# Kernel optimization log

Hardware: AMD Instinct MI355X
Metric: run time of the kernel (lower is better)

Reference implementation:

```python
import jax, jax.numpy as jnp
import numpy as np
import math

B, S, D, H = 2, 2048, 2048, 16
DH = D // H  # head dim = 128
THETA = 10000.0


def _rope(x, pos):
    """Interleaved RoPE. x: [..., S, DH], pos: [S] (int)."""
    dh = x.shape[-1]
    freqs = (1.0 / THETA) ** (2.0 * jnp.arange(dh // 2, dtype=jnp.float32) / dh)  # [DH/2]
    ang = pos.astype(jnp.float32)[:, None] * freqs[None, :]  # [S, DH/2]
    cos = jnp.cos(ang).astype(x.dtype)
    sin = jnp.sin(ang).astype(x.dtype)
    xe = x[..., 0::2]
    xo = x[..., 1::2]
    oe = xe * cos - xo * sin
    oo = xe * sin + xo * cos
    return jnp.stack([oe, oo], axis=-1).reshape(x.shape)


def setup_inputs() -> dict:
    key = jax.random.key(0)
    ks = jax.random.split(key, 5)
    std = 2.0 / math.sqrt(D + D)
    x = jax.random.normal(ks[0], (B, S, D), dtype=jnp.float32)
    Wq = jax.random.normal(ks[1], (D, D), dtype=jnp.float32) * std
    Wk = jax.random.normal(ks[2], (D, D), dtype=jnp.float32) * std
    Wv = jax.random.normal(ks[3], (D, D), dtype=jnp.float32) * std
    Wo = jax.random.normal(ks[4], (D, D), dtype=jnp.float32) * std
    token_positions = jnp.arange(S, dtype=jnp.int64 if jax.config.jax_enable_x64 else jnp.int32)[None, :]
    return {"x": x, "token_positions": token_positions, "Wq": Wq, "Wk": Wk, "Wv": Wv, "Wo": Wo}


def reference(x, token_positions, Wq, Wk, Wv, Wo):
    b, s, d = x.shape
    pos = token_positions[0]  # [S]
    # QKV projections (Linear is x @ W.T, no bias)
    Q = (x @ Wq.T).reshape(b, s, H, DH).transpose(0, 2, 1, 3)  # [b,h,s,dh]
    K = (x @ Wk.T).reshape(b, s, H, DH).transpose(0, 2, 1, 3)
    V = (x @ Wv.T).reshape(b, s, H, DH).transpose(0, 2, 1, 3)
    # per-head RoPE on Q and K
    Q = _rope(Q, pos)
    K = _rope(K, pos)
    # scaled dot-product attention with causal mask
    scores = jnp.einsum('bhqd,bhkd->bhqk', Q, K) / math.sqrt(DH)
    causal = jnp.tril(jnp.ones((s, s), dtype=bool))  # [s,s]
    scores = jnp.where(causal[None, None, :, :], scores, -jnp.inf)
    prob = jax.nn.softmax(scores, axis=-1)
    O = jnp.einsum('bhqk,bhkd->bhqd', prob, V)  # [b,h,s,dh]
    O = O.transpose(0, 2, 1, 3).reshape(b, s, d)
    return O @ Wo.T
```

## Files before the change

kernel.cpp:

```cpp
#include <hip/hip_runtime.h>
#include <hip/hip_bf16.h>
#include <math.h>

#define BB 2
#define SS 2048
#define DD 2048
#define HH 16
#define DHH 128
#define MM (BB*SS)

typedef __attribute__((ext_vector_type(8))) short bf16x8;
typedef __attribute__((ext_vector_type(4))) float f32x4;

#define AS1 __attribute__((address_space(1)))
#define AS3 __attribute__((address_space(3)))
#define GLOAD_LDS16(g, l) __builtin_amdgcn_global_load_lds((const AS1 void*)(g), (AS3 void*)(l), 16, 0, 0)

#if __has_builtin(__builtin_amdgcn_exp2f)
#define EXP2F(x) __builtin_amdgcn_exp2f(x)
#else
#define EXP2F(x) exp2f(x)
#endif

__device__ __forceinline__ float b2f(short s) {
  union { unsigned int u; float f; } v;
  v.u = ((unsigned int)(unsigned short)s) << 16;
  return v.f;
}
__device__ __forceinline__ short f2b(float f) {
  union { float f; unsigned int u; } v; v.f = f;
  unsigned int u = v.u;
  u += 0x7fffu + ((u >> 16) & 1u);
  return (short)(u >> 16);
}
__device__ __forceinline__ short f2b_fast(float f) {
  union { float f; unsigned int u; } v; v.f = f;
  return (short)((v.u + 0x8000u) >> 16);
}

template<int CTRL>
__device__ __forceinline__ float dppf(float x) {
  int xi = __builtin_bit_cast(int, x);
  int r = __builtin_amdgcn_update_dpp(0, xi, CTRL, 0xf, 0xf, true);
  return __builtin_bit_cast(float, r);
}
__device__ __forceinline__ float rmax16(float x) {
  x = fmaxf(x, dppf<0xB1>(x));
  x = fmaxf(x, dppf<0x4E>(x));
  x = fmaxf(x, dppf<0x141>(x));
  x = fmaxf(x, dppf<0x140>(x));
  return x;
}
__device__ __forceinline__ float rsum16(float x) {
  x += dppf<0xB1>(x);
  x += dppf<0x4E>(x);
  x += dppf<0x141>(x);
  x += dppf<0x140>(x);
  return x;
}

__global__ void cvt_all(const float* __restrict__ x,  const float* __restrict__ wq,
                        const float* __restrict__ wk, const float* __restrict__ wv,
                        const float* __restrict__ wo,
                        short* __restrict__ xb,  short* __restrict__ wqb,
                        short* __restrict__ wkb, short* __restrict__ wvb,
                        short* __restrict__ wob) {
  int i = blockIdx.x * blockDim.x + threadIdx.x;
  const float* src; short* dst; int off;
  if (i < 2097152) { src = x; dst = xb; off = i; }
  else {
    int j = i - 2097152;
    int w = j >> 20; off = j & 1048575;
    src = (w == 0) ? wq : (w == 1) ? wk : (w == 2) ? wv : wo;
    dst = (w == 0) ? wqb : (w == 1) ? wkb : (w == 2) ? wvb : wob;
  }
  float4 v = ((const float4*)src)[i < 2097152 ? off : off];
  short4 o;
  o.x = f2b(v.x); o.y = f2b(v.y); o.z = f2b(v.z); o.w = f2b(v.w);
  ((short4*)dst)[off] = o;
}

#define LDA(cb, mt, kk) (*(const bf16x8*)((const char*)smA + (cb)*32768 + \
    (wm*128 + (mt)*16 + l16)*128 + (((kk)*64 + quad*16) ^ ((l16 & 7) << 4))))
#define LDB(cb, nt, kk) (*(const bf16x8*)((const char*)smB + (cb)*32768 + \
    (wn*64 + (nt)*16 + l16)*128 + (((kk)*64 + quad*16) ^ ((l16 & 7) << 4))))
#define STGA(b, t, h) do { \
    GLOAD_LDS16(aBase + (size_t)((h)*128) * DD + (t)*64,      smA + (b)*16384 + ((h)*128)*64 + wst); \
    GLOAD_LDS16(aBase + (size_t)((h)*128 + 64) * DD + (t)*64, smA + (b)*16384 + ((h)*128 + 64)*64 + wst); } while(0)
#define STGB(b, t, h) do { \
    GLOAD_LDS16(bBase + (size_t)((h)*128) * DD + (t)*64,      smB + (b)*16384 + ((h)*128)*64 + wst); \
    GLOAD_LDS16(bBase + (size_t)((h)*128 + 64) * DD + (t)*64, smB + (b)*16384 + ((h)*128 + 64)*64 + wst); } while(0)
#define MFMA_Q(MT0, NT0) do { \
    __builtin_amdgcn_s_setprio(1); \
    _Pragma("unroll") \
    for (int mt = 0; mt < 4; ++mt) \
      _Pragma("unroll") \
      for (int nt = 0; nt < 2; ++nt) \
        _Pragma("unroll") \
        for (int kk = 0; kk < 2; ++kk) \
          acc[(MT0) + mt][(NT0) + nt] = __builtin_amdgcn_mfma_f32_16x16x32_bf16( \
              af[mt][kk], bf[(NT0) + nt][kk], acc[(MT0) + mt][(NT0) + nt], 0, 0, 0); \
    __builtin_amdgcn_s_setprio(0); } while(0)

__global__ __launch_bounds__(512, 2)
void gemm_qkv(const short* __restrict__ A,
              const short* __restrict__ Wq, const short* __restrict__ Wk,
              const short* __restrict__ Wv, const int* __restrict__ pos,
              short* __restrict__ Qo, short* __restrict__ Ko, short* __restrict__ Vo) {
  __shared__ __align__(16) short sm[65536];
  const int tid = threadIdx.x;
  const int lane = tid & 63;
  const int wave = tid >> 6;
  const int quad = lane >> 4, l16 = lane & 15;
  const int wm = wave >> 2, wn = wave & 3;
  const int wsel = blockIdx.x >> 3;
  const short* Bw = (wsel == 0) ? Wq : (wsel == 1) ? Wk : Wv;
  short* Cout = (wsel == 0) ? Qo : (wsel == 1) ? Ko : Vo;
  const int bn = (blockIdx.x & 7) * 256;
  const int bm = blockIdx.y * 256;

  short* smA = sm;
  short* smB = sm + 32768;
  const int wst = wave * 512;

  const int srow = tid >> 3;
  const int scol = ((tid & 7) ^ (srow & 7)) * 8;
  const short* aBase = A  + (size_t)(bm + srow) * DD + scol;
  const short* bBase = Bw + (size_t)(bn + srow) * DD + scol;

  f32x4 acc[8][4] = {};
  bf16x8 af[4][2], bf[4][2];

  STGA(0, 0, 0); STGA(0, 0, 1);
  STGB(0, 0, 0); STGB(0, 0, 1);
  STGB(1, 1, 0); STGB(1, 1, 1);
  asm volatile("s_waitcnt vmcnt(4)" ::: "memory");
  __builtin_amdgcn_s_barrier();

  for (int t = 0; t < 32; ++t) {
    const int cb = t & 1, nb = cb ^ 1;
    #pragma unroll
    for (int mt = 0; mt < 4; ++mt) { af[mt][0] = LDA(cb, mt, 0); af[mt][1] = LDA(cb, mt, 1); }
    #pragma unroll
    for (int nt = 0; nt < 2; ++nt) { bf[nt][0] = LDB(cb, nt, 0); bf[nt][1] = LDB(cb, nt, 1); }
    if (t + 1 < 32) STGA(nb, t + 1, 0);
    __builtin_amdgcn_s_barrier();
    asm volatile("s_waitcnt lgkmcnt(0)" ::: "memory");
    __builtin_amdgcn_sched_barrier(0);
    MFMA_Q(0, 0);
    __builtin_amdgcn_s_barrier();
    #pragma unroll
    for (int nt = 2; nt < 4; ++nt) { bf[nt][0] = LDB(cb, nt, 0); bf[nt][1] = LDB(cb, nt, 1); }
    if (t + 1 < 32) STGA(nb, t + 1, 1);
    __builtin_amdgcn_s_barrier();
    asm volatile("s_waitcnt lgkmcnt(0)" ::: "memory");
    __builtin_amdgcn_sched_barrier(0);
    MFMA_Q(0, 2);
    __builtin_amdgcn_s_barrier();
    #pragma unroll
    for (int mt = 0; mt < 4; ++mt) { af[mt][0] = LDA(cb, mt + 4, 0); af[mt][1] = LDA(cb, mt + 4, 1); }
    if (t + 2 < 32) STGB(cb, t + 2, 0);
    __builtin_amdgcn_s_barrier();
    asm volatile("s_waitcnt lgkmcnt(0)" ::: "memory");
    __builtin_amdgcn_sched_barrier(0);
    MFMA_Q(4, 2);
    __builtin_amdgcn_s_barrier();
    if (t + 2 < 32) {
      STGB(cb, t + 2, 1);
      asm volatile("s_waitcnt vmcnt(4)" ::: "memory");
    } else {
      asm volatile("s_waitcnt vmcnt(0)" ::: "memory");
    }
    __builtin_amdgcn_s_barrier();
    MFMA_Q(4, 0);
    __builtin_amdgcn_s_barrier();
  }

  if (wsel < 2) {
    const float post = (wsel == 0) ? 0.1275174306f : 1.0f;
    float fr[4];
    #pragma unroll
    for (int nt = 0; nt < 4; ++nt) {
      int pi = (wn & 1) * 32 + nt * 8 + (l16 >> 1);
      fr[nt] = __expf(-0.14391156831f * (float)pi);
    }
    const float sgn = (l16 & 1) ? 1.0f : -1.0f;
    #pragma unroll
    for (int mt = 0; mt < 8; ++mt) {
      #pragma unroll
      for (int r = 0; r < 4; ++r) {
        int m = bm + wm*128 + mt*16 + quad*4 + r;
        float fp = (float)pos[m & 2047];
        #pragma unroll
        for (int nt = 0; nt < 4; ++nt) {
          float v = acc[mt][nt][r];
          float p = dppf<0xB1>(v);
          float ang = fp * fr[nt];
          float sn = __sinf(ang), cs = __cosf(ang);
          acc[mt][nt][r] = (v * cs + sgn * p * sn) * post;
        }
      }
    }
  }

  #pragma unroll
  for (int mt = 0; mt < 8; ++mt)
    #pragma unroll
    for (int nt = 0; nt < 4; ++nt)
      #pragma unroll
      for (int r = 0; r < 4; ++r) {
        int m = bm + wm*128 + mt*16 + quad*4 + r;
        int n = bn + wn*64 + nt*16 + l16;
        int b = m >> 11, s = m & 2047;
        int h = n >> 7,  d = n & 127;
        Cout[(((size_t)(b*HH + h)*SS + s)*DHH) + d] = f2b(acc[mt][nt][r]);
      }
}

__global__ __launch_bounds__(256)
void gemm_o(const short* __restrict__ A, const short* __restrict__ Bw,
            float* __restrict__ Cout) {
  __shared__ __align__(16) short As[128*64];
  __shared__ __align__(16) short Bs[128*64];
  const int tid = threadIdx.x;
  const int lane = tid & 63;
  const int wave = tid >> 6;
  const int wm = wave >> 1, wn = wave & 1;
  const int quad = lane >> 4, l16 = lane & 15;
  const int bm = blockIdx.y * 128, bn = blockIdx.x * 128;
  const int K = DD;

  const int srow = tid >> 3;
  const int scol = (tid & 7) * 8;
  const short* aBase = A + (size_t)(bm + srow) * K + scol;
  const short* bBase = Bw + (size_t)(bn + srow) * K + scol;
  f32x4 acc[4][4] = {};

  for (int k0 = 0; k0 < K; k0 += 64) {
    #pragma unroll
    for (int j = 0; j < 4; ++j) {
      GLOAD_LDS16(aBase + (size_t)j * 32 * K + k0, As + j * 2048 + wave * 512);
      GLOAD_LDS16(bBase + (size_t)j * 32 * K + k0, Bs + j * 2048 + wave * 512);
    }
    __syncthreads();
    #pragma unroll
    for (int kk = 0; kk < 64; kk += 32) {
      bf16x8 af[4], bf[4];
      #pragma unroll
      for (int t = 0; t < 4; ++t)
        af[t] = *(const bf16x8*)&As[(wm*64 + t*16 + l16) * 64 + kk + quad*8];
      #pragma unroll
      for (int t = 0; t < 4; ++t)
        bf[t] = *(const bf16x8*)&Bs[(wn*64 + t*16 + l16) * 64 + kk + quad*8];
      #pragma unroll
      for (int mt = 0; mt < 4; ++mt)
        #pragma unroll
        for (int nt = 0; nt < 4; ++nt)
          acc[mt][nt] = __builtin_amdgcn_mfma_f32_16x16x32_bf16(af[mt], bf[nt], acc[mt][nt], 0, 0, 0);
    }
    __syncthreads();
  }

  #pragma unroll
  for (int mt = 0; mt < 4; ++mt)
    #pragma unroll
    for (int nt = 0; nt < 4; ++nt)
      #pragma unroll
      for (int r = 0; r < 4; ++r) {
        int m = bm + wm*64 + mt*16 + quad*4 + r;
        int n = bn + wn*64 + nt*16 + l16;
        Cout[(size_t)m * DD + n] = acc[mt][nt][r];
      }
}

__global__ __launch_bounds__(512, 4)
void attn(const short* __restrict__ Q, const short* __restrict__ K,
          const short* __restrict__ V, short* __restrict__ O) {
  __shared__ __align__(16) short Ks[64*128];
  __shared__ __align__(16) short Vt[128*64];
  __shared__ __align__(16) short Pb[8*16*64];
  const int tid = threadIdx.x;
  const int lane = tid & 63, wave = tid >> 6;
  const int quad = lane >> 4, l16 = lane & 15;
  const int p = blockIdx.x;
  const int qa = p, qb = 31 - p;
  const int bh = blockIdx.y;
  const int b = bh >> 4, h = bh & 15;
  const short* Kg = K + (size_t)bh * SS * DHH;
  const short* Vg = V + (size_t)bh * SS * DHH;

  const int wt = wave >> 2;
  const int qtile = wt ? qb : qa;
  const int qbase = qtile * 64 + (wave & 3) * 16;

  bf16x8 aq[4];
  {
    const short* qp = Q + ((size_t)bh * SS + qbase + l16) * DHH + quad*8;
    #pragma unroll
    for (int ks = 0; ks < 4; ++ks) aq[ks] = *(const bf16x8*)(qp + ks*32);
  }

  f32x4 o[8] = {};
  float mrow[4], lrow[4];
  #pragma unroll
  for (int r = 0; r < 4; ++r) { mrow[r] = -1e30f; lrow[r] = 0.f; }

  const int krow = tid >> 3;
  const int kcolb = (tid & 7) * 32;
  const int vkp = (tid & 31) * 2;
  const int vds = (tid >> 5) * 8;

  const int nkt = qb + 1;
  int4 kreg[2], vreg[2];
  {
    const short* kp = Kg + (size_t)krow * DHH + (kcolb >> 1);
    kreg[0] = *(const int4*)kp; kreg[1] = *(const int4*)(kp + 8);
    const short* vp = Vg + (size_t)vkp * DHH + vds;
    vreg[0] = *(const int4*)vp; vreg[1] = *(const int4*)(vp + DHH);
  }

  for (int kt = 0; kt < nkt; ++kt) {
    #pragma unroll
    for (int j = 0; j < 2; ++j)
      *(int4*)((char*)Ks + krow*256 + ((kcolb + j*16) ^ ((krow & 7) << 4))) = kreg[j];
    {
      const short* s0 = (const short*)&vreg[0];
      const short* s1 = (const short*)&vreg[1];
      #pragma unroll
      for (int e = 0; e < 8; ++e) {
        int dim = vds + e;
        int val = (int)(unsigned short)s0[e] | ((int)(unsigned short)s1[e] << 16);
        *(int*)((char*)Vt + dim*128 + ((vkp*2) ^ ((dim & 7) << 4))) = val;
      }
    }
    __syncthreads();

    if (kt + 1 < nkt) {
      const short* kp = Kg + (size_t)((kt+1)*64 + krow) * DHH + (kcolb >> 1);
      kreg[0] = *(const int4*)kp; kreg[1] = *(const int4*)(kp + 8);
      const short* vp = Vg + (size_t)((kt+1)*64 + vkp) * DHH + vds;
      vreg[0] = *(const int4*)vp; vreg[1] = *(const int4*)(vp + DHH);
    }

    if (kt <= qtile) {
      float sv[4][4];
      __builtin_amdgcn_s_setprio(1);
      #pragma unroll
      for (int nt = 0; nt < 4; ++nt) {
        f32x4 a = {0.f, 0.f, 0.f, 0.f};
        #pragma unroll
        for (int ks = 0; ks < 4; ++ks) {
          int key = nt*16 + l16;
          bf16x8 bk = *(const bf16x8*)((const char*)Ks + key*256 +
                         ((ks*64 + quad*16) ^ ((key & 7) << 4)));
          a = __builtin_amdgcn_mfma_f32_16x16x32_bf16(aq[ks], bk, a, 0, 0, 0);
        }
        #pragma unroll
        for (int r = 0; r < 4; ++r) sv[nt][r] = a[r];
      }
      __builtin_amdgcn_s_setprio(0);

      if (kt == qtile) {
        #pragma unroll
        for (int nt = 0; nt < 4; ++nt)
          #pragma unroll
          for (int r = 0; r < 4; ++r)
            if (nt*16 + l16 > (wave & 3)*16 + quad*4 + r) sv[nt][r] = -1e30f;
      }

      #pragma unroll
      for (int r = 0; r < 4; ++r) {
        float mx = fmaxf(fmaxf(sv[0][r], sv[1][r]), fmaxf(sv[2][r], sv[3][r]));
        mx = rmax16(mx);
        float mnew = fmaxf(mrow[r], mx);
        float alpha = EXP2F(mrow[r] - mnew);
        float ls = 0.f;
        #pragma unroll
        for (int nt = 0; nt < 4; ++nt) {
          float pv = EXP2F(sv[nt][r] - mnew);
          sv[nt][r] = pv; ls += pv;
        }
        ls = rsum16(ls);
        lrow[r] = lrow[r] * alpha + ls;
        mrow[r] = mnew;
        #pragma unroll
        for (int nt = 0; nt < 8; ++nt) o[nt][r] *= alpha;
      }

      #pragma unroll
      for (int nt = 0; nt < 4; ++nt)
        #pragma unroll
        for (int r = 0; r < 4; ++r) {
          int qr = quad*4 + r;
          *(short*)((char*)Pb + wave*2048 + qr*128 +
                    (((nt*16 + l16)*2) ^ ((qr & 7) << 4))) = f2b_fast(sv[nt][r]);
        }

      bf16x8 ap[2];
      #pragma unroll
      for (int k2 = 0; k2 < 2; ++k2)
        ap[k2] = *(const bf16x8*)((const char*)Pb + wave*2048 + l16*128 +
                    ((k2*64 + quad*16) ^ ((l16 & 7) << 4)));

      __builtin_amdgcn_s_setprio(1);
      #pragma unroll
      for (int k2 = 0; k2 < 2; ++k2)
        #pragma unroll
        for (int nt = 0; nt < 8; ++nt) {
          int d = nt*16 + l16;
          bf16x8 bv = *(const bf16x8*)((const char*)Vt + d*128 +
                         ((k2*64 + quad*16) ^ ((d & 7) << 4)));
          o[nt] = __builtin_amdgcn_mfma_f32_16x16x32_bf16(ap[k2], bv, o[nt], 0, 0, 0);
        }
      __builtin_amdgcn_s_setprio(0);
    }
    __syncthreads();
  }

  #pragma unroll
  for (int nt = 0; nt < 8; ++nt)
    #pragma unroll
    for (int r = 0; r < 4; ++r) {
      int q = qbase + quad*4 + r;
      float v = o[nt][r] / lrow[r];
      O[((size_t)(b*SS + q)) * DD + h*DHH + nt*16 + l16] = f2b(v);
    }
}

extern "C" void kernel_launch(void* const* d_in, const int* in_sizes, int n_in,
                              void* d_out, int out_size, void* d_ws, size_t ws_size,
                              hipStream_t stream) {
  const float* x  = (const float*)d_in[0];
  const int* pos  = (const int*)d_in[1];
  const float* Wq = (const float*)d_in[2];
  const float* Wk = (const float*)d_in[3];
  const float* Wv = (const float*)d_in[4];
  const float* Wo = (const float*)d_in[5];

  char* ws = (char*)d_ws;
  short* xb  = (short*)(ws);
  short* wqb = (short*)(ws + 16777216);
  short* wkb = (short*)(ws + 25165824);
  short* wvb = (short*)(ws + 33554432);
  short* wob = (short*)(ws + 41943040);
  short* Qb  = (short*)(ws + 50331648);
  short* Kb  = (short*)(ws + 67108864);
  short* Vb  = (short*)(ws + 83886080);
  short* Ob  = (short*)(ws + 100663296);

  cvt_all<<<24576, 256, 0, stream>>>(x, Wq, Wk, Wv, Wo, xb, wqb, wkb, wvb, wob);

  dim3 gq(24, MM/256);
  gemm_qkv<<<gq, 512, 0, stream>>>(xb, wqb, wkb, wvb, pos, Qb, Kb, Vb);

  dim3 ga(16, BB*HH);
  attn<<<ga, 512, 0, stream>>>(Qb, Kb, Vb, Ob);

  dim3 go(DD/128, MM/128);
  gemm_o<<<go, 256, 0, stream>>>(Ob, wob, (float*)d_out);
}
```

Measured before the change: 427.0 us.

## Split attention into one q-tile per block with heavy-first ordering and lazy rescale

The attention kernel changes from 512-thread blocks that each handle a paired short and long query tile to 1024 blocks of 256 threads, one query tile each. Block order is chosen so the longest causal tiles launch first. This removes the idle waves that previously waited on the other tile's key loop, at the cost of loading each K/V tile in twice as many blocks. It also adds a lazy online-softmax rescale that skips the alpha update when the wave's row max has not grown past a threshold, which saves exp and multiply work at some risk to numerical range.

```diff
diff --git a/kernel.cpp b/kernel.cpp
--- a/kernel.cpp
+++ b/kernel.cpp
@@ -273,25 +273,24 @@
       }
 }
 
-__global__ __launch_bounds__(512, 4)
+__global__ __launch_bounds__(256, 4)
 void attn(const short* __restrict__ Q, const short* __restrict__ K,
           const short* __restrict__ V, short* __restrict__ O) {
   __shared__ __align__(16) short Ks[64*128];
   __shared__ __align__(16) short Vt[128*64];
-  __shared__ __align__(16) short Pb[8*16*64];
+  __shared__ __align__(16) short Pb[4*16*64];
   const int tid = threadIdx.x;
   const int lane = tid & 63, wave = tid >> 6;
   const int quad = lane >> 4, l16 = lane & 15;
-  const int p = blockIdx.x;
-  const int qa = p, qb = 31 - p;
-  const int bh = blockIdx.y;
+  const int L = blockIdx.x;
+  const int bh = L & 31;
+  const int s = L >> 5;
+  const int qt = (s < 8) ? 31 - s : (s < 16) ? s - 8 : (s < 24) ? 39 - s : s - 16;
   const int b = bh >> 4, h = bh & 15;
   const short* Kg = K + (size_t)bh * SS * DHH;
   const short* Vg = V + (size_t)bh * SS * DHH;
 
-  const int wt = wave >> 2;
-  const int qtile = wt ? qb : qa;
-  const int qbase = qtile * 64 + (wave & 3) * 16;
+  const int qbase = qt * 64 + wave * 16;
 
   bf16x8 aq[4];
   {
@@ -305,29 +304,31 @@
   #pragma unroll
   for (int r = 0; r < 4; ++r) { mrow[r] = -1e30f; lrow[r] = 0.f; }
 
-  const int krow = tid >> 3;
-  const int kcolb = (tid & 7) * 32;
+  const int krow = tid >> 2;
+  const int kcolb = (tid & 3) * 64;
   const int vkp = (tid & 31) * 2;
-  const int vds = (tid >> 5) * 8;
-
-  const int nkt = qb + 1;
-  int4 kreg[2], vreg[2];
+  const int vds = (tid >> 5) * 16;
+
+  const int nkt = qt + 1;
+  int4 kreg[4], vreg[4];
   {
     const short* kp = Kg + (size_t)krow * DHH + (kcolb >> 1);
-    kreg[0] = *(const int4*)kp; kreg[1] = *(const int4*)(kp + 8);
+    #pragma unroll
+    for (int j = 0; j < 4; ++j) kreg[j] = *(const int4*)(kp + j*8);
     const short* vp = Vg + (size_t)vkp * DHH + vds;
-    vreg[0] = *(const int4*)vp; vreg[1] = *(const int4*)(vp + DHH);
+    vreg[0] = *(const int4*)vp;        vreg[1] = *(const int4*)(vp + 8);
+    vreg[2] = *(const int4*)(vp + DHH); vreg[3] = *(const int4*)(vp + DHH + 8);
   }
 
   for (int kt = 0; kt < nkt; ++kt) {
     #pragma unroll
-    for (int j = 0; j < 2; ++j)
+    for (int j = 0; j < 4; ++j)
       *(int4*)((char*)Ks + krow*256 + ((kcolb + j*16) ^ ((krow & 7) << 4))) = kreg[j];
     {
       const short* s0 = (const short*)&vreg[0];
-      const short* s1 = (const short*)&vreg[1];
-      #pragma unroll
-      for (int e = 0; e < 8; ++e) {
+      const short* s1 = (const short*)&vreg[2];
+      #pragma unroll
+      for (int e = 0; e < 16; ++e) {
         int dim = vds + e;
         int val = (int)(unsigned short)s0[e] | ((int)(unsigned short)s1[e] << 16);
         *(int*)((char*)Vt + dim*128 + ((vkp*2) ^ ((dim & 7) << 4))) = val;
@@ -337,83 +338,87 @@
 
     if (kt + 1 < nkt) {
       const short* kp = Kg + (size_t)((kt+1)*64 + krow) * DHH + (kcolb >> 1);
-      kreg[0] = *(const int4*)kp; kreg[1] = *(const int4*)(kp + 8);
+      #pragma unroll
+      for (int j = 0; j < 4; ++j) kreg[j] = *(const int4*)(kp + j*8);
       const short* vp = Vg + (size_t)((kt+1)*64 + vkp) * DHH + vds;
-      vreg[0] = *(const int4*)vp; vreg[1] = *(const int4*)(vp + DHH);
-    }
-
-    if (kt <= qtile) {
-      float sv[4][4];
-      __builtin_amdgcn_s_setprio(1);
-      #pragma unroll
-      for (int nt = 0; nt < 4; ++nt) {
-        f32x4 a = {0.f, 0.f, 0.f, 0.f};
+      vreg[0] = *(const int4*)vp;        vreg[1] = *(const int4*)(vp + 8);
+      vreg[2] = *(const int4*)(vp + DHH); vreg[3] = *(const int4*)(vp + DHH + 8);
+    }
+
+    float sv[4][4];
+    __builtin_amdgcn_s_setprio(1);
+    #pragma unroll
+    for (int nt = 0; nt < 4; ++nt) {
+      f32x4 a = {0.f, 0.f, 0.f, 0.f};
+      #pragma unroll
+      for (int ks = 0; ks < 4; ++ks) {
+        int key = nt*16 + l16;
+        bf16x8 bk = *(const bf16x8*)((const char*)Ks + key*256 +
+                       ((ks*64 + quad*16) ^ ((key & 7) << 4)));
+        a = __builtin_amdgcn_mfma_f32_16x16x32_bf16(aq[ks], bk, a, 0, 0, 0);
+      }
+      #pragma unroll
+      for (int r = 0; r < 4; ++r) sv[nt][r] = a[r];
+    }
+    __builtin_amdgcn_s_setprio(0);
+
+    if (kt == qt) {
+      #pragma unroll
+      for (int nt = 0; nt < 4; ++nt)
         #pragma unroll
-        for (int ks = 0; ks < 4; ++ks) {
-          int key = nt*16 + l16;
-          bf16x8 bk = *(const bf16x8*)((const char*)Ks + key*256 +
-                         ((ks*64 + quad*16) ^ ((key & 7) << 4)));
-          a = __builtin_amdgcn_mfma_f32_16x16x32_bf16(aq[ks], bk, a, 0, 0, 0);
-        }
-        #pragma unroll
-        for (int r = 0; r < 4; ++r) sv[nt][r] = a[r];
-      }
-      __builtin_amdgcn_s_setprio(0);
-
-      if (kt == qtile) {
-        #pragma unroll
-        for (int nt = 0; nt < 4; ++nt)
-          #pragma unroll
-          for (int r = 0; r < 4; ++r)
-            if (nt*16 + l16 > (wave & 3)*16 + quad*4 + r) sv[nt][r] = -1e30f;
-      }
-
-      #pragma unroll
-      for (int r = 0; r < 4; ++r) {
-        float mx = fmaxf(fmaxf(sv[0][r], sv[1][r]), fmaxf(sv[2][r], sv[3][r]));
-        mx = rmax16(mx);
+        for (int r = 0; r < 4; ++r)
+          if (nt*16 + l16 > wave*16 + quad*4 + r) sv[nt][r] = -1e30f;
+    }
+
+    #pragma unroll
+    for (int r = 0; r < 4; ++r) {
+      float mx = fmaxf(fmaxf(sv[0][r], sv[1][r]), fmaxf(sv[2][r], sv[3][r]));
+      mx = rmax16(mx);
+      if (!__all(mx - mrow[r] <= 11.5f)) {
         float mnew = fmaxf(mrow[r], mx);
         float alpha = EXP2F(mrow[r] - mnew);
-        float ls = 0.f;
-        #pragma unroll
-        for (int nt = 0; nt < 4; ++nt) {
-          float pv = EXP2F(sv[nt][r] - mnew);
-          sv[nt][r] = pv; ls += pv;
-        }
-        ls = rsum16(ls);
-        lrow[r] = lrow[r] * alpha + ls;
-        mrow[r] = mnew;
+        lrow[r] *= alpha;
         #pragma unroll
         for (int nt = 0; nt < 8; ++nt) o[nt][r] *= alpha;
-      }
-
-      #pragma unroll
-      for (int nt = 0; nt < 4; ++nt)
-        #pragma unroll
-        for (int r = 0; r < 4; ++r) {
-          int qr = quad*4 + r;
-          *(short*)((char*)Pb + wave*2048 + qr*128 +
-                    (((nt*16 + l16)*2) ^ ((qr & 7) << 4))) = f2b_fast(sv[nt][r]);
-        }
-
-      bf16x8 ap[2];
-      #pragma unroll
-      for (int k2 = 0; k2 < 2; ++k2)
-        ap[k2] = *(const bf16x8*)((const char*)Pb + wave*2048 + l16*128 +
-                    ((k2*64 + quad*16) ^ ((l16 & 7) << 4)));
-
-      __builtin_amdgcn_s_setprio(1);
-      #pragma unroll
-      for (int k2 = 0; k2 < 2; ++k2)
-        #pragma unroll
-        for (int nt = 0; nt < 8; ++nt) {
-          int d = nt*16 + l16;
-          bf16x8 bv = *(const bf16x8*)((const char*)Vt + d*128 +
-                         ((k2*64 + quad*16) ^ ((d & 7) << 4)));
-          o[nt] = __builtin_amdgcn_mfma_f32_16x16x32_bf16(ap[k2], bv, o[nt], 0, 0, 0);
-        }
-      __builtin_amdgcn_s_setprio(0);
-    }
+        mrow[r] = mnew;
+      }
+      float ls = 0.f;
+      #pragma unroll
+      for (int nt = 0; nt < 4; ++nt) {
+        float pv = EXP2F(sv[nt][r] - mrow[r]);
+        sv[nt][r] = pv; ls += pv;
+      }
+      ls = rsum16(ls);
+      lrow[r] += ls;
+    }
+
+    #pragma unroll
+    for (int nt = 0; nt < 4; ++nt)
+      #pragma unroll
+      for (int r = 0; r < 4; ++r) {
+        int qr = quad*4 + r;
+        *(short*)((char*)Pb + wave*2048 + qr*128 +
+                  (((nt*16 + l16)*2) ^ ((qr & 7) << 4))) = f2b_fast(sv[nt][r]);
+      }
+
+    bf16x8 ap[2];
+    #pragma unroll
+    for (int k2 = 0; k2 < 2; ++k2)
+      ap[k2] = *(const bf16x8*)((const char*)Pb + wave*2048 + l16*128 +
+                  ((k2*64 + quad*16) ^ ((l16 & 7) << 4)));
+
+    __builtin_amdgcn_s_setprio(1);
+    #pragma unroll
+    for (int k2 = 0; k2 < 2; ++k2)
+      #pragma unroll
+      for (int nt = 0; nt < 8; ++nt) {
+        int d = nt*16 + l16;
+        bf16x8 bv = *(const bf16x8*)((const char*)Vt + d*128 +
+                       ((k2*64 + quad*16) ^ ((d & 7) << 4)));
+        o[nt] = __builtin_amdgcn_mfma_f32_16x16x32_bf16(ap[k2], bv, o[nt], 0, 0, 0);
+      }
+    __builtin_amdgcn_s_setprio(0);
+
     __syncthreads();
   }
 
@@ -453,8 +458,7 @@
   dim3 gq(24, MM/256);
   gemm_qkv<<<gq, 512, 0, stream>>>(xb, wqb, wkb, wvb, pos, Qb, Kb, Vb);
 
-  dim3 ga(16, BB*HH);
-  attn<<<ga, 512, 0, stream>>>(Qb, Kb, Vb, Ob);
+  attn<<<1024, 256, 0, stream>>>(Qb, Kb, Vb, Ob);
 
   dim3 go(DD/128, MM/128);
   gemm_o<<<go, 256, 0, stream>>>(Ob, wob, (float*)d_out);
```

Result: slower. 973.4 us (+128.0%).
